# Optimization experiments

Hardware: AMD Instinct MI355X
Metric: run time of the kernel (lower is better)

## Reference

```python
import jax, jax.numpy as jnp
import numpy as np
import math

B, T, E = 2, 2048, 2048
G, QPG, D = 4, 4, 128  # kv groups, queries per group, head dim (G*QPG*D == E)


def sinusoidal_pe(t, d, dtype):
    pos = jnp.arange(t, dtype=jnp.float32)[:, None]            # [T,1]
    i = jnp.arange(0, d, 2, dtype=jnp.float32)                 # [D/2]
    inv_freq = jnp.exp(-(jnp.log(10000.0) * i / d))            # [D/2]
    ang = pos * inv_freq                                       # [T,D/2]
    pe = jnp.zeros((t, d), dtype=jnp.float32)
    pe = pe.at[:, 0::2].set(jnp.sin(ang)).at[:, 1::2].set(jnp.cos(ang))
    return pe.astype(dtype)


def setup_inputs() -> dict:
    key = jax.random.key(0)
    ks = jax.random.split(key, 6)
    s = lambda fan_in: 1.0 / math.sqrt(fan_in)
    return {
        "x":   jax.random.normal(ks[0], (B, T, E), dtype=jnp.float32),
        "wq":  jax.random.uniform(ks[1], (E, G * QPG * D), jnp.float32, -s(E), s(E)),
        "bq":  jax.random.uniform(ks[2], (G * QPG * D,), jnp.float32, -s(E), s(E)),
        "wkv": jax.random.uniform(ks[3], (E, 2 * G * D), jnp.float32, -s(E), s(E)),
        "bkv": jax.random.uniform(ks[4], (2 * G * D,), jnp.float32, -s(E), s(E)),
        "wo":  jax.random.uniform(ks[5], (G * QPG * D, E), jnp.float32, -s(G * QPG * D), s(G * QPG * D)),
    }


def reference(x, wq, bq, wkv, bkv, wo):
    b, t, e = x.shape
    # projections
    q = (x @ wq + bq).reshape(b, t, G, QPG, D).transpose(0, 2, 3, 1, 4)   # [B,G,QPG,T,D]
    kv = (x @ wkv + bkv).reshape(b, t, G, 1, 2 * D).transpose(0, 2, 3, 1, 4)  # [B,G,1,T,2D]
    k, v = kv[..., :D], kv[..., D:]                                       # [B,G,1,T,D]
    # inline additive sinusoidal positional embedding on q and k
    pe = sinusoidal_pe(t, D, x.dtype)                                     # [T,D]
    q = q + pe
    k = k + pe
    # scores: [B,G,QPG,T,T] (kv head axis k has size 1, summed out)
    scores = jnp.einsum('bgqtd,bgksd->bgqts', q, k) / math.sqrt(D)
    causal = jnp.tril(jnp.ones((t, t), dtype=bool))                       # [T,T]
    scores = jnp.where(causal, scores, -jnp.inf)
    probs = jax.nn.softmax(scores, axis=-1)
    out = jnp.einsum('bgqts,bgksd->btgqd', probs, v).reshape(b, t, G * QPG * D)
    return out @ wo
```

## Files before the change

kernel.cpp:

```cpp
#include <hip/hip_runtime.h>
#include <stdint.h>

typedef __bf16 bf16;
typedef __bf16 bf16x4 __attribute__((ext_vector_type(4)));
typedef __bf16 bf16x8 __attribute__((ext_vector_type(8)));
typedef float floatx4 __attribute__((ext_vector_type(4)));

#define B_   2
#define T_   2048
#define E_   2048
#define G_   4
#define QPG_ 4
#define D_   128
#define H_   16
#define NQ   2048
#define NKV  1024
#define NQKV 3072
#define M_   4096

__device__ __forceinline__ void gload_lds16(const void* g, void* l) {
  __builtin_amdgcn_global_load_lds(
      (__attribute__((address_space(1))) unsigned int*)g,
      (__attribute__((address_space(3))) unsigned int*)l,
      16, 0, 0);
}

__device__ __forceinline__ int swz_stage_col(int lane) {
  return (((lane & 3) ^ ((lane >> 2) & 3) ^ ((lane >> 4) & 3))) * 8;
}


__global__ void cast_f32_bf16(const float* __restrict__ in, bf16* __restrict__ out, int n4) {
  int i = blockIdx.x * blockDim.x + threadIdx.x;
  if (i < n4) {
    float4 v = ((const float4*)in)[i];
    bf16x4 o = {(bf16)v.x, (bf16)v.y, (bf16)v.z, (bf16)v.w};
    ((bf16x4*)out)[i] = o;
  }
}

__global__ void transpose_cast(const float* __restrict__ in, bf16* __restrict__ out,
                               int R, int C, int out_stride) {
  __shared__ float tile[64][65];
  int r0 = blockIdx.x * 64, c0 = blockIdx.y * 64;
  int tx = threadIdx.x & 63, ty = threadIdx.x >> 6;
  for (int i = ty; i < 64; i += 4)
    tile[i][tx] = in[(size_t)(r0 + i) * C + c0 + tx];
  __syncthreads();
  for (int i = ty; i < 64; i += 4)
    out[(size_t)(c0 + i) * out_stride + r0 + tx] = (bf16)tile[tx][i];
}

__global__ void concat_bias(const float* __restrict__ bq, const float* __restrict__ bkv,
                            float* __restrict__ out) {
  int i = blockIdx.x * 256 + threadIdx.x;
  out[i] = (i < NQ) ? bq[i] : bkv[i - NQ];
}


template <int OUT_BF16, int HAS_BIAS>
__global__ __launch_bounds__(256, 2) void gemm_bt(
    const bf16* __restrict__ A, const bf16* __restrict__ Bt,
    const float* __restrict__ bias, void* __restrict__ Cout,
    int M, int N, int K) {
  __shared__ __align__(16) bf16 As[128 * 32];
  __shared__ __align__(16) bf16 Bs[128 * 32];
  const int tid = threadIdx.x;
  const int wave = tid >> 6, lane = tid & 63;
  const int quad = lane >> 4, c = lane & 15;
  const int m0 = blockIdx.x * 128, n0 = blockIdx.y * 128;
  const int wr = (wave >> 1) * 64, wc = (wave & 1) * 64;
  const int xsl = ((quad ^ (c & 3) ^ ((c >> 2) & 3)) & 3) * 8;

  floatx4 acc[4][4];
#pragma unroll
  for (int i = 0; i < 4; ++i)
#pragma unroll
    for (int j = 0; j < 4; ++j) acc[i][j] = (floatx4){0.f, 0.f, 0.f, 0.f};

  const int srow = wave * 32 + (lane >> 2);
  const int scol = swz_stage_col(lane);
  const bf16* Ap = A + (size_t)(m0 + srow) * K + scol;
  const bf16* Bp = Bt + (size_t)(n0 + srow) * K + scol;

  for (int k0 = 0; k0 < K; k0 += 32) {
#pragma unroll
    for (int ch = 0; ch < 2; ++ch) {
      gload_lds16(Ap + (size_t)ch * 16 * K + k0, &As[(wave * 2 + ch) * 512]);
      gload_lds16(Bp + (size_t)ch * 16 * K + k0, &Bs[(wave * 2 + ch) * 512]);
    }
    __syncthreads();
    bf16x8 af[4], bfr[4];
#pragma unroll
    for (int i = 0; i < 4; ++i) {
      af[i]  = *(const bf16x8*)(&As[(wr + i * 16 + c) * 32 + xsl]);
      bfr[i] = *(const bf16x8*)(&Bs[(wc + i * 16 + c) * 32 + xsl]);
    }
#pragma unroll
    for (int mi = 0; mi < 4; ++mi)
#pragma unroll
      for (int ni = 0; ni < 4; ++ni)
        acc[mi][ni] = __builtin_amdgcn_mfma_f32_16x16x32_bf16(af[mi], bfr[ni], acc[mi][ni], 0, 0, 0);
    __syncthreads();
  }

  float bv[4] = {0.f, 0.f, 0.f, 0.f};
  if (HAS_BIAS) {
#pragma unroll
    for (int ni = 0; ni < 4; ++ni) bv[ni] = bias[n0 + wc + ni * 16 + c];
  }
#pragma unroll
  for (int mi = 0; mi < 4; ++mi) {
#pragma unroll
    for (int ni = 0; ni < 4; ++ni) {
      const int col = n0 + wc + ni * 16 + c;
#pragma unroll
      for (int r = 0; r < 4; ++r) {
        const int row = m0 + wr + mi * 16 + quad * 4 + r;
        float v = acc[mi][ni][r] + bv[ni];
        if (OUT_BF16)
          ((bf16*)Cout)[(size_t)row * N + col] = (bf16)v;
        else
          ((float*)Cout)[(size_t)row * N + col] = v;
      }
    }
  }
}


__device__ __forceinline__ float pe_val(int t, int d) {
  int i2 = d & ~1;
  float inv = __expf(-9.210340371976184f * (float)i2 * (1.0f / 128.0f));
  float ang = (float)t * inv;
  return (d & 1) ? cosf(ang) : sinf(ang);
}

__global__ void scatter_qk(const bf16* __restrict__ qkv,
                           bf16* __restrict__ Qb, bf16* __restrict__ Kb) {
  const int row = blockIdx.x;
  const int b = row >> 11, t = row & 2047;
  const int tid = threadIdx.x;
  const int d = tid & 127;
  const float scale = 0.12751745f;
  const float pe = pe_val(t, d);
  for (int h = tid >> 7; h < H_; h += 2) {
    float q = (float)qkv[(size_t)row * NQKV + h * 128 + d] + pe;
    Qb[((size_t)(b * H_ + h) * T_ + t) * D_ + d] = (bf16)(q * scale);
  }
  for (int g = tid >> 7; g < G_; g += 2) {
    float k = (float)qkv[(size_t)row * NQKV + NQ + g * 256 + d] + pe;
    Kb[((size_t)(b * G_ + g) * T_ + t) * D_ + d] = (bf16)k;
  }
}

__global__ void build_vt(const bf16* __restrict__ qkv, bf16* __restrict__ Vt) {
  __shared__ float tile[64][65];
  int t0 = blockIdx.x * 64, d0 = blockIdx.y * 64;
  int bg = blockIdx.z, b = bg >> 2, g = bg & 3;
  const bf16* src = qkv + (size_t)b * T_ * NQKV + NQ + g * 256 + 128;
  bf16* dst = Vt + (size_t)bg * D_ * T_;
  int tx = threadIdx.x & 63, ty = threadIdx.x >> 6;
  for (int i = ty; i < 64; i += 4)
    tile[i][tx] = (float)src[(size_t)(t0 + i) * NQKV + d0 + tx];
  __syncthreads();
  for (int i = ty; i < 64; i += 4)
    dst[(size_t)(d0 + i) * T_ + t0 + tx] = (bf16)tile[tx][i];
}


__global__ __launch_bounds__(256, 4) void flash_attn(
    const bf16* __restrict__ Qb, const bf16* __restrict__ Kb,
    const bf16* __restrict__ Vt, bf16* __restrict__ Ob) {
  const int qt = (blockIdx.x + blockIdx.y) & 31;
  const int bh = blockIdx.y;
  const int b = bh >> 4, h = bh & 15, g = h >> 2;
  const int tid = threadIdx.x;
  const int wave = tid >> 6, lane = tid & 63;
  const int quad = lane >> 4, c = lane & 15;
  const int xsl = ((quad ^ (c & 3) ^ ((c >> 2) & 3)) & 3) * 8;

  __shared__ __align__(16) bf16 Ks[2][4][32 * 32];
  __shared__ __align__(16) bf16 Vs[2][4][32 * 32];
  __shared__ __align__(16) bf16 Pq[4][16 * 40];

  const int q0 = qt * 64;
  const bf16* Qbase = Qb + ((size_t)(b * H_ + h) * T_ + q0 + wave * 16 + c) * D_;
  bf16x8 qf[4];
#pragma unroll
  for (int ks = 0; ks < 4; ++ks)
    qf[ks] = *(const bf16x8*)(Qbase + ks * 32 + quad * 8);

  floatx4 acc[8];
#pragma unroll
  for (int i = 0; i < 8; ++i) acc[i] = (floatx4){0.f, 0.f, 0.f, 0.f};
  float rsum[4] = {0.f, 0.f, 0.f, 0.f};

  const bf16* Kg = Kb + (size_t)(b * G_ + g) * T_ * D_;
  const bf16* Vg = Vt + (size_t)(b * G_ + g) * D_ * T_;
  const int slr = lane >> 2;
  const int slc = swz_stage_col(lane);
  const int nt = 2 * qt + 2;

  auto stage = [&](int t, int bu) {
    const int k0 = t * 32;
#pragma unroll
    for (int hh = 0; hh < 2; ++hh)
      gload_lds16(Kg + (size_t)(k0 + hh * 16 + slr) * D_ + wave * 32 + slc,
                  &Ks[bu][wave][hh * 16 * 32]);
#pragma unroll
    for (int hh = 0; hh < 2; ++hh)
      gload_lds16(Vg + (size_t)(wave * 32 + hh * 16 + slr) * T_ + k0 + slc,
                  &Vs[bu][wave][hh * 16 * 32]);
  };

  stage(0, 0);

  for (int j = 0; j < nt; ++j) {
    __syncthreads();
    if (j + 1 < nt) stage(j + 1, (j + 1) & 1);

    const bf16* Kt  = &Ks[j & 1][0][0];
    const bf16* Vtl = &Vs[j & 1][0][0];

    floatx4 s[2];
    s[0] = (floatx4){0.f, 0.f, 0.f, 0.f};
    s[1] = (floatx4){0.f, 0.f, 0.f, 0.f};
#pragma unroll
    for (int ks = 0; ks < 4; ++ks)
#pragma unroll
      for (int n = 0; n < 2; ++n) {
        bf16x8 kf = *(const bf16x8*)(Kt + ks * 1024 + (n * 16 + c) * 32 + xsl);
        s[n] = __builtin_amdgcn_mfma_f32_16x16x32_bf16(qf[ks], kf, s[n], 0, 0, 0);
      }

    if (j >= 2 * qt) {
      const int colb = j * 32;
      const int rowb = q0 + wave * 16 + quad * 4;
#pragma unroll
      for (int n = 0; n < 2; ++n)
#pragma unroll
        for (int r = 0; r < 4; ++r)
          if (colb + n * 16 + c > rowb + r) s[n][r] = -1e30f;
    }

    float pvv[2][4];
#pragma unroll
    for (int n = 0; n < 2; ++n)
#pragma unroll
      for (int r = 0; r < 4; ++r) {
        float p = exp2f(s[n][r]);
        pvv[n][r] = p;
        rsum[r] += p;
      }

    bf16* Pw = &Pq[wave][0];
#pragma unroll
    for (int n = 0; n < 2; ++n)
#pragma unroll
      for (int r = 0; r < 4; ++r)
        Pw[(quad * 4 + r) * 40 + n * 16 + c] = (bf16)pvv[n][r];

    bf16x8 pf = *(const bf16x8*)(&Pw[c * 40 + quad * 8]);

#pragma unroll
    for (int nd = 0; nd < 8; ++nd) {
      bf16x8 vf = *(const bf16x8*)(Vtl + (nd >> 1) * 1024 + ((nd & 1) * 16 + c) * 32 + xsl);
      acc[nd] = __builtin_amdgcn_mfma_f32_16x16x32_bf16(pf, vf, acc[nd], 0, 0, 0);
    }
  }

#pragma unroll
  for (int off = 1; off < 16; off <<= 1)
#pragma unroll
    for (int r = 0; r < 4; ++r) rsum[r] += __shfl_xor(rsum[r], off);

  float linv[4];
#pragma unroll
  for (int r = 0; r < 4; ++r) linv[r] = 1.f / rsum[r];
#pragma unroll
  for (int nd = 0; nd < 8; ++nd) {
    const int dd = nd * 16 + c;
#pragma unroll
    for (int r = 0; r < 4; ++r) {
      const int trow = q0 + wave * 16 + quad * 4 + r;
      Ob[((size_t)(b * T_ + trow)) * NQ + h * D_ + dd] = (bf16)(acc[nd][r] * linv[r]);
    }
  }
}


extern "C" void kernel_launch(void* const* d_in, const int* in_sizes, int n_in,
                              void* d_out, int out_size, void* d_ws, size_t ws_size,
                              hipStream_t stream) {
  const float* x   = (const float*)d_in[0];
  const float* wq  = (const float*)d_in[1];
  const float* bq  = (const float*)d_in[2];
  const float* wkv = (const float*)d_in[3];
  const float* bkv = (const float*)d_in[4];
  const float* wo  = (const float*)d_in[5];
  float* out = (float*)d_out;

  char* p = (char*)d_ws;
  bf16* xb    = (bf16*)p; p += (size_t)M_ * E_ * 2;
  bf16* wqkvT = (bf16*)p; p += (size_t)NQKV * E_ * 2;
  bf16* woT   = (bf16*)p; p += (size_t)E_ * NQ * 2;
  float* biasq = (float*)p; p += 16384;
  bf16* qkv   = (bf16*)p; p += (size_t)M_ * NQKV * 2;
  bf16* Qb    = (bf16*)p; p += (size_t)B_ * H_ * T_ * D_ * 2;
  bf16* Kb    = (bf16*)p; p += (size_t)B_ * G_ * T_ * D_ * 2;
  bf16* Vtb   = (bf16*)p; p += (size_t)B_ * G_ * D_ * T_ * 2;
  bf16* Ob    = (bf16*)p; p += (size_t)M_ * NQ * 2;

  cast_f32_bf16<<<(M_ * E_ / 4) / 256, 256, 0, stream>>>(x, xb, M_ * E_ / 4);
  transpose_cast<<<dim3(E_ / 64, E_ / 64), 256, 0, stream>>>(wq, wqkvT, E_, E_, E_);
  transpose_cast<<<dim3(E_ / 64, NKV / 64), 256, 0, stream>>>(wkv, wqkvT + (size_t)NQ * E_, E_, NKV, E_);
  transpose_cast<<<dim3(E_ / 64, E_ / 64), 256, 0, stream>>>(wo, woT, NQ, E_, NQ);
  concat_bias<<<NQKV / 256, 256, 0, stream>>>(bq, bkv, biasq);

  gemm_bt<1, 1><<<dim3(M_ / 128, NQKV / 128), 256, 0, stream>>>(xb, wqkvT, biasq, qkv, M_, NQKV, E_);
  scatter_qk<<<M_, 256, 0, stream>>>(qkv, Qb, Kb);
  build_vt<<<dim3(T_ / 64, D_ / 64, B_ * G_), 256, 0, stream>>>(qkv, Vtb);
  flash_attn<<<dim3(T_ / 64, B_ * H_), 256, 0, stream>>>(Qb, Kb, Vtb, Ob);
  gemm_bt<0, 0><<<dim3(M_ / 128, E_ / 128), 256, 0, stream>>>(Ob, woT, nullptr, out, M_, E_, NQ);
}
```

Before: 328.1 us.

## Use two-wave attention blocks with 32 query rows per wave and balanced tile order

The flash attention kernel now runs 128-thread blocks where each wave handles two 16-row query sub-tiles. Each K/V fragment read from LDS then feeds twice as many MFMAs, which cuts LDS traffic per flop. Causal work is balanced by ordering query tiles so heavy and light tiles alternate across the 1D grid. Waves skip compute on key tiles past their diagonal. The cost is more registers per wave, fewer waves per block to hide latency, and each wave now issues twice the staging loads.

```diff
diff --git a/kernel.cpp b/kernel.cpp
--- a/kernel.cpp
+++ b/kernel.cpp
@@ -168,49 +168,61 @@
 }
 
 
-__global__ __launch_bounds__(256, 4) void flash_attn(
+__global__ __launch_bounds__(128, 2) void flash_attn(
     const bf16* __restrict__ Qb, const bf16* __restrict__ Kb,
     const bf16* __restrict__ Vt, bf16* __restrict__ Ob) {
-  const int qt = (blockIdx.x + blockIdx.y) & 31;
-  const int bh = blockIdx.y;
+  const int i = blockIdx.x;
+  const int grp = i >> 8, jj = i & 255;
+  const int bh = ((grp & 1) << 4) | (jj >> 4);
+  const int q4 = jj & 15;
+  const int qt = (grp == 0) ? q4 : (grp == 1) ? 31 - q4 : (grp == 2) ? 16 + q4 : 15 - q4;
   const int b = bh >> 4, h = bh & 15, g = h >> 2;
   const int tid = threadIdx.x;
-  const int wave = tid >> 6, lane = tid & 63;
+  const int w = tid >> 6, lane = tid & 63;
   const int quad = lane >> 4, c = lane & 15;
   const int xsl = ((quad ^ (c & 3) ^ ((c >> 2) & 3)) & 3) * 8;
 
   __shared__ __align__(16) bf16 Ks[2][4][32 * 32];
   __shared__ __align__(16) bf16 Vs[2][4][32 * 32];
-  __shared__ __align__(16) bf16 Pq[4][16 * 40];
+  __shared__ __align__(16) bf16 Pq[2][2][16 * 40];
 
   const int q0 = qt * 64;
-  const bf16* Qbase = Qb + ((size_t)(b * H_ + h) * T_ + q0 + wave * 16 + c) * D_;
-  bf16x8 qf[4];
-#pragma unroll
-  for (int ks = 0; ks < 4; ++ks)
-    qf[ks] = *(const bf16x8*)(Qbase + ks * 32 + quad * 8);
-
-  floatx4 acc[8];
-#pragma unroll
-  for (int i = 0; i < 8; ++i) acc[i] = (floatx4){0.f, 0.f, 0.f, 0.f};
-  float rsum[4] = {0.f, 0.f, 0.f, 0.f};
+  bf16x8 qf[2][4];
+#pragma unroll
+  for (int hf = 0; hf < 2; ++hf) {
+    const bf16* Qbase = Qb + ((size_t)(b * H_ + h) * T_ + q0 + w * 32 + hf * 16 + c) * D_;
+#pragma unroll
+    for (int ks = 0; ks < 4; ++ks)
+      qf[hf][ks] = *(const bf16x8*)(Qbase + ks * 32 + quad * 8);
+  }
+
+  floatx4 acc[2][8];
+#pragma unroll
+  for (int hf = 0; hf < 2; ++hf)
+#pragma unroll
+    for (int nd = 0; nd < 8; ++nd) acc[hf][nd] = (floatx4){0.f, 0.f, 0.f, 0.f};
+  float rsum[2][4] = {{0.f, 0.f, 0.f, 0.f}, {0.f, 0.f, 0.f, 0.f}};
 
   const bf16* Kg = Kb + (size_t)(b * G_ + g) * T_ * D_;
   const bf16* Vg = Vt + (size_t)(b * G_ + g) * D_ * T_;
   const int slr = lane >> 2;
   const int slc = swz_stage_col(lane);
   const int nt = 2 * qt + 2;
+  const int amax = 2 * qt + w;
 
   auto stage = [&](int t, int bu) {
     const int k0 = t * 32;
 #pragma unroll
-    for (int hh = 0; hh < 2; ++hh)
-      gload_lds16(Kg + (size_t)(k0 + hh * 16 + slr) * D_ + wave * 32 + slc,
-                  &Ks[bu][wave][hh * 16 * 32]);
-#pragma unroll
-    for (int hh = 0; hh < 2; ++hh)
-      gload_lds16(Vg + (size_t)(wave * 32 + hh * 16 + slr) * T_ + k0 + slc,
-                  &Vs[bu][wave][hh * 16 * 32]);
+    for (int cc = 0; cc < 2; ++cc) {
+      const int ch = w + cc * 2;
+#pragma unroll
+      for (int hh = 0; hh < 2; ++hh) {
+        gload_lds16(Kg + (size_t)(k0 + hh * 16 + slr) * D_ + ch * 32 + slc,
+                    &Ks[bu][ch][hh * 16 * 32]);
+        gload_lds16(Vg + (size_t)(ch * 32 + hh * 16 + slr) * T_ + k0 + slc,
+                    &Vs[bu][ch][hh * 16 * 32]);
+      }
+    }
   };
 
   stage(0, 0);
@@ -218,72 +230,82 @@
   for (int j = 0; j < nt; ++j) {
     __syncthreads();
     if (j + 1 < nt) stage(j + 1, (j + 1) & 1);
+    if (j > amax) continue;
 
     const bf16* Kt  = &Ks[j & 1][0][0];
     const bf16* Vtl = &Vs[j & 1][0][0];
 
-    floatx4 s[2];
-    s[0] = (floatx4){0.f, 0.f, 0.f, 0.f};
-    s[1] = (floatx4){0.f, 0.f, 0.f, 0.f};
+    floatx4 s[2][2];
+#pragma unroll
+    for (int hf = 0; hf < 2; ++hf)
+#pragma unroll
+      for (int n = 0; n < 2; ++n) s[hf][n] = (floatx4){0.f, 0.f, 0.f, 0.f};
 #pragma unroll
     for (int ks = 0; ks < 4; ++ks)
 #pragma unroll
       for (int n = 0; n < 2; ++n) {
         bf16x8 kf = *(const bf16x8*)(Kt + ks * 1024 + (n * 16 + c) * 32 + xsl);
-        s[n] = __builtin_amdgcn_mfma_f32_16x16x32_bf16(qf[ks], kf, s[n], 0, 0, 0);
-      }
-
-    if (j >= 2 * qt) {
+        s[0][n] = __builtin_amdgcn_mfma_f32_16x16x32_bf16(qf[0][ks], kf, s[0][n], 0, 0, 0);
+        s[1][n] = __builtin_amdgcn_mfma_f32_16x16x32_bf16(qf[1][ks], kf, s[1][n], 0, 0, 0);
+      }
+
+    if (j == amax) {
       const int colb = j * 32;
-      const int rowb = q0 + wave * 16 + quad * 4;
+#pragma unroll
+      for (int hf = 0; hf < 2; ++hf) {
+        const int rowb = q0 + w * 32 + hf * 16 + quad * 4;
+#pragma unroll
+        for (int n = 0; n < 2; ++n)
+#pragma unroll
+          for (int r = 0; r < 4; ++r)
+            if (colb + n * 16 + c > rowb + r) s[hf][n][r] = -1e30f;
+      }
+    }
+
+#pragma unroll
+    for (int hf = 0; hf < 2; ++hf) {
+      bf16* Pw = &Pq[w][hf][0];
 #pragma unroll
       for (int n = 0; n < 2; ++n)
 #pragma unroll
-        for (int r = 0; r < 4; ++r)
-          if (colb + n * 16 + c > rowb + r) s[n][r] = -1e30f;
-    }
-
-    float pvv[2][4];
-#pragma unroll
-    for (int n = 0; n < 2; ++n)
-#pragma unroll
-      for (int r = 0; r < 4; ++r) {
-        float p = exp2f(s[n][r]);
-        pvv[n][r] = p;
-        rsum[r] += p;
-      }
-
-    bf16* Pw = &Pq[wave][0];
-#pragma unroll
-    for (int n = 0; n < 2; ++n)
-#pragma unroll
-      for (int r = 0; r < 4; ++r)
-        Pw[(quad * 4 + r) * 40 + n * 16 + c] = (bf16)pvv[n][r];
-
-    bf16x8 pf = *(const bf16x8*)(&Pw[c * 40 + quad * 8]);
+        for (int r = 0; r < 4; ++r) {
+          float p = exp2f(s[hf][n][r]);
+          rsum[hf][r] += p;
+          Pw[(quad * 4 + r) * 40 + n * 16 + c] = (bf16)p;
+        }
+    }
+
+    bf16x8 pf0 = *(const bf16x8*)(&Pq[w][0][c * 40 + quad * 8]);
+    bf16x8 pf1 = *(const bf16x8*)(&Pq[w][1][c * 40 + quad * 8]);
 
 #pragma unroll
     for (int nd = 0; nd < 8; ++nd) {
       bf16x8 vf = *(const bf16x8*)(Vtl + (nd >> 1) * 1024 + ((nd & 1) * 16 + c) * 32 + xsl);
-      acc[nd] = __builtin_amdgcn_mfma_f32_16x16x32_bf16(pf, vf, acc[nd], 0, 0, 0);
+      acc[0][nd] = __builtin_amdgcn_mfma_f32_16x16x32_bf16(pf0, vf, acc[0][nd], 0, 0, 0);
+      acc[1][nd] = __builtin_amdgcn_mfma_f32_16x16x32_bf16(pf1, vf, acc[1][nd], 0, 0, 0);
     }
   }
 
 #pragma unroll
   for (int off = 1; off < 16; off <<= 1)
 #pragma unroll
-    for (int r = 0; r < 4; ++r) rsum[r] += __shfl_xor(rsum[r], off);
-
-  float linv[4];
-#pragma unroll
-  for (int r = 0; r < 4; ++r) linv[r] = 1.f / rsum[r];
-#pragma unroll
-  for (int nd = 0; nd < 8; ++nd) {
-    const int dd = nd * 16 + c;
-#pragma unroll
-    for (int r = 0; r < 4; ++r) {
-      const int trow = q0 + wave * 16 + quad * 4 + r;
-      Ob[((size_t)(b * T_ + trow)) * NQ + h * D_ + dd] = (bf16)(acc[nd][r] * linv[r]);
+    for (int hf = 0; hf < 2; ++hf)
+#pragma unroll
+      for (int r = 0; r < 4; ++r) rsum[hf][r] += __shfl_xor(rsum[hf][r], off);
+
+#pragma unroll
+  for (int hf = 0; hf < 2; ++hf) {
+    float linv[4];
+#pragma unroll
+    for (int r = 0; r < 4; ++r) linv[r] = 1.f / rsum[hf][r];
+#pragma unroll
+    for (int nd = 0; nd < 8; ++nd) {
+      const int dd = nd * 16 + c;
+#pragma unroll
+      for (int r = 0; r < 4; ++r) {
+        const int trow = q0 + w * 32 + hf * 16 + quad * 4 + r;
+        Ob[((size_t)(b * T_ + trow)) * NQ + h * D_ + dd] = (bf16)(acc[hf][nd][r] * linv[r]);
+      }
     }
   }
 }
@@ -320,6 +342,6 @@
   gemm_bt<1, 1><<<dim3(M_ / 128, NQKV / 128), 256, 0, stream>>>(xb, wqkvT, biasq, qkv, M_, NQKV, E_);
   scatter_qk<<<M_, 256, 0, stream>>>(qkv, Qb, Kb);
   build_vt<<<dim3(T_ / 64, D_ / 64, B_ * G_), 256, 0, stream>>>(qkv, Vtb);
-  flash_attn<<<dim3(T_ / 64, B_ * H_), 256, 0, stream>>>(Qb, Kb, Vtb, Ob);
+  flash_attn<<<1024, 128, 0, stream>>>(Qb, Kb, Vtb, Ob);
   gemm_bt<0, 0><<<dim3(M_ / 128, E_ / 128), 256, 0, stream>>>(Ob, woT, nullptr, out, M_, E_, NQ);
 }
```

Result: slower. 336.0 us (+2.4%).

## Split KV range across two wave groups in flash attention with LDS merge

Applied to the files above, without the earlier changes.

The attention block grows to 512 threads. Two groups of four waves each process half of the causal KV tiles for the same 64-query tile, and their partial accumulators and row sums are merged through shared memory at the end. The grid becomes 1D with heaviest query tiles scheduled first, which aims to shorten the critical path and improve load balance. This costs more LDS (about 74KB per block), reduces occupancy, adds an extra sync and merge step, and leaves some waves idle on uneven splits.

```diff
diff --git a/kernel.cpp b/kernel.cpp
--- a/kernel.cpp
+++ b/kernel.cpp
@@ -168,23 +168,26 @@
 }
 
 
-__global__ __launch_bounds__(256, 4) void flash_attn(
+__global__ __launch_bounds__(512, 4) void flash_attn(
     const bf16* __restrict__ Qb, const bf16* __restrict__ Kb,
     const bf16* __restrict__ Vt, bf16* __restrict__ Ob) {
-  const int qt = (blockIdx.x + blockIdx.y) & 31;
-  const int bh = blockIdx.y;
-  const int b = bh >> 4, h = bh & 15, g = h >> 2;
+  const int i = blockIdx.x;
+  const int qt = 31 - (i >> 5);
+  const int bh = i & 31;
+  const int b = bh >> 4, h = bh & 15, g2 = h >> 2;
   const int tid = threadIdx.x;
   const int wave = tid >> 6, lane = tid & 63;
+  const int grp = wave >> 2, w4 = wave & 3;
   const int quad = lane >> 4, c = lane & 15;
   const int xsl = ((quad ^ (c & 3) ^ ((c >> 2) & 3)) & 3) * 8;
 
-  __shared__ __align__(16) bf16 Ks[2][4][32 * 32];
-  __shared__ __align__(16) bf16 Vs[2][4][32 * 32];
-  __shared__ __align__(16) bf16 Pq[4][16 * 40];
+  __shared__ __align__(16) char smem[75776];
+  bf16* Ks = (bf16*)smem;
+  bf16* Vs = (bf16*)(smem + 32768);
+  bf16* Pq = (bf16*)(smem + 65536);
 
   const int q0 = qt * 64;
-  const bf16* Qbase = Qb + ((size_t)(b * H_ + h) * T_ + q0 + wave * 16 + c) * D_;
+  const bf16* Qbase = Qb + ((size_t)(b * H_ + h) * T_ + q0 + w4 * 16 + c) * D_;
   bf16x8 qf[4];
 #pragma unroll
   for (int ks = 0; ks < 4; ++ks)
@@ -192,35 +195,38 @@
 
   floatx4 acc[8];
 #pragma unroll
-  for (int i = 0; i < 8; ++i) acc[i] = (floatx4){0.f, 0.f, 0.f, 0.f};
+  for (int nd = 0; nd < 8; ++nd) acc[nd] = (floatx4){0.f, 0.f, 0.f, 0.f};
   float rsum[4] = {0.f, 0.f, 0.f, 0.f};
 
-  const bf16* Kg = Kb + (size_t)(b * G_ + g) * T_ * D_;
-  const bf16* Vg = Vt + (size_t)(b * G_ + g) * D_ * T_;
+  const bf16* Kg = Kb + (size_t)(b * G_ + g2) * T_ * D_;
+  const bf16* Vg = Vt + (size_t)(b * G_ + g2) * D_ * T_;
   const int slr = lane >> 2;
   const int slc = swz_stage_col(lane);
-  const int nt = 2 * qt + 2;
+  const int ng = qt + 1;
+  const int jbase = grp * ng;
+  const int amax = 2 * qt + (w4 >> 1);
 
   auto stage = [&](int t, int bu) {
     const int k0 = t * 32;
-#pragma unroll
-    for (int hh = 0; hh < 2; ++hh)
-      gload_lds16(Kg + (size_t)(k0 + hh * 16 + slr) * D_ + wave * 32 + slc,
-                  &Ks[bu][wave][hh * 16 * 32]);
-#pragma unroll
-    for (int hh = 0; hh < 2; ++hh)
-      gload_lds16(Vg + (size_t)(wave * 32 + hh * 16 + slr) * T_ + k0 + slc,
-                  &Vs[bu][wave][hh * 16 * 32]);
+    bf16* kd = Ks + ((grp * 2 + bu) * 4 + w4) * 1024;
+    bf16* vd = Vs + ((grp * 2 + bu) * 4 + w4) * 1024;
+#pragma unroll
+    for (int hh = 0; hh < 2; ++hh) {
+      gload_lds16(Kg + (size_t)(k0 + hh * 16 + slr) * D_ + w4 * 32 + slc, kd + hh * 512);
+      gload_lds16(Vg + (size_t)(w4 * 32 + hh * 16 + slr) * T_ + k0 + slc, vd + hh * 512);
+    }
   };
 
-  stage(0, 0);
-
-  for (int j = 0; j < nt; ++j) {
+  stage(jbase, 0);
+
+  for (int jg = 0; jg < ng; ++jg) {
     __syncthreads();
-    if (j + 1 < nt) stage(j + 1, (j + 1) & 1);
-
-    const bf16* Kt  = &Ks[j & 1][0][0];
-    const bf16* Vtl = &Vs[j & 1][0][0];
+    if (jg + 1 < ng) stage(jbase + jg + 1, (jg + 1) & 1);
+    const int j = jbase + jg;
+    if (j > amax) continue;
+
+    const bf16* Kt  = Ks + (grp * 2 + (jg & 1)) * 4096;
+    const bf16* Vtl = Vs + (grp * 2 + (jg & 1)) * 4096;
 
     floatx4 s[2];
     s[0] = (floatx4){0.f, 0.f, 0.f, 0.f};
@@ -233,9 +239,9 @@
         s[n] = __builtin_amdgcn_mfma_f32_16x16x32_bf16(qf[ks], kf, s[n], 0, 0, 0);
       }
 
-    if (j >= 2 * qt) {
+    if (j == amax) {
       const int colb = j * 32;
-      const int rowb = q0 + wave * 16 + quad * 4;
+      const int rowb = q0 + w4 * 16 + quad * 4;
 #pragma unroll
       for (int n = 0; n < 2; ++n)
 #pragma unroll
@@ -243,22 +249,15 @@
           if (colb + n * 16 + c > rowb + r) s[n][r] = -1e30f;
     }
 
-    float pvv[2][4];
+    bf16* Pw = Pq + wave * 640;
 #pragma unroll
     for (int n = 0; n < 2; ++n)
 #pragma unroll
       for (int r = 0; r < 4; ++r) {
         float p = exp2f(s[n][r]);
-        pvv[n][r] = p;
         rsum[r] += p;
-      }
-
-    bf16* Pw = &Pq[wave][0];
-#pragma unroll
-    for (int n = 0; n < 2; ++n)
-#pragma unroll
-      for (int r = 0; r < 4; ++r)
-        Pw[(quad * 4 + r) * 40 + n * 16 + c] = (bf16)pvv[n][r];
+        Pw[(quad * 4 + r) * 40 + n * 16 + c] = (bf16)p;
+      }
 
     bf16x8 pf = *(const bf16x8*)(&Pw[c * 40 + quad * 8]);
 
@@ -274,17 +273,53 @@
 #pragma unroll
     for (int r = 0; r < 4; ++r) rsum[r] += __shfl_xor(rsum[r], off);
 
+  __syncthreads();
+  float* mrg = (float*)smem;
+  float* mrs = (float*)(smem + 34816);
+  const int row16 = w4 * 16 + quad * 4;
+
+  if (grp == 0) {
+#pragma unroll
+    for (int nd2 = 0; nd2 < 4; ++nd2)
+#pragma unroll
+      for (int r = 0; r < 4; ++r)
+        mrg[(row16 + r) * 68 + nd2 * 16 + c] = acc[4 + nd2][r];
+  } else {
+#pragma unroll
+    for (int nd2 = 0; nd2 < 4; ++nd2)
+#pragma unroll
+      for (int r = 0; r < 4; ++r)
+        mrg[(64 + row16 + r) * 68 + nd2 * 16 + c] = acc[nd2][r];
+  }
+  if (c == 0) {
+#pragma unroll
+    for (int r = 0; r < 4; ++r) mrs[grp * 64 + row16 + r] = rsum[r];
+  }
+  __syncthreads();
+
+  const int og = grp ^ 1;
   float linv[4];
 #pragma unroll
-  for (int r = 0; r < 4; ++r) linv[r] = 1.f / rsum[r];
-#pragma unroll
-  for (int nd = 0; nd < 8; ++nd) {
-    const int dd = nd * 16 + c;
-#pragma unroll
-    for (int r = 0; r < 4; ++r) {
-      const int trow = q0 + wave * 16 + quad * 4 + r;
-      Ob[((size_t)(b * T_ + trow)) * NQ + h * D_ + dd] = (bf16)(acc[nd][r] * linv[r]);
-    }
+  for (int r = 0; r < 4; ++r) linv[r] = 1.f / (rsum[r] + mrs[og * 64 + row16 + r]);
+
+  if (grp == 0) {
+#pragma unroll
+    for (int nd2 = 0; nd2 < 4; ++nd2)
+#pragma unroll
+      for (int r = 0; r < 4; ++r) {
+        float o = acc[nd2][r] + mrg[(64 + row16 + r) * 68 + nd2 * 16 + c];
+        const int trow = q0 + row16 + r;
+        Ob[((size_t)(b * T_ + trow)) * NQ + h * D_ + nd2 * 16 + c] = (bf16)(o * linv[r]);
+      }
+  } else {
+#pragma unroll
+    for (int nd2 = 0; nd2 < 4; ++nd2)
+#pragma unroll
+      for (int r = 0; r < 4; ++r) {
+        float o = acc[4 + nd2][r] + mrg[(row16 + r) * 68 + nd2 * 16 + c];
+        const int trow = q0 + row16 + r;
+        Ob[((size_t)(b * T_ + trow)) * NQ + h * D_ + (4 + nd2) * 16 + c] = (bf16)(o * linv[r]);
+      }
   }
 }
 
@@ -320,6 +355,6 @@
   gemm_bt<1, 1><<<dim3(M_ / 128, NQKV / 128), 256, 0, stream>>>(xb, wqkvT, biasq, qkv, M_, NQKV, E_);
   scatter_qk<<<M_, 256, 0, stream>>>(qkv, Qb, Kb);
   build_vt<<<dim3(T_ / 64, D_ / 64, B_ * G_), 256, 0, stream>>>(qkv, Vtb);
-  flash_attn<<<dim3(T_ / 64, B_ * H_), 256, 0, stream>>>(Qb, Kb, Vtb, Ob);
+  flash_attn<<<1024, 512, 0, stream>>>(Qb, Kb, Vtb, Ob);
   gemm_bt<0, 0><<<dim3(M_ / 128, E_ / 128), 256, 0, stream>>>(Ob, woT, nullptr, out, M_, E_, NQ);
 }
```

Measured after the change: 325.0 us. Within noise of the previous version (-0.9%).
